# Performance work log

Measured on AMD Instinct MI355X. Metric: run time of the kernel, lower is better.

## Reference

```python
import jax, jax.numpy as jnp
import numpy as np

NUM_JOINTS = 24
V = 6890
# standard SMPL kinematic tree (parent of joint i); index 0 is the root
PARENTS = [-1, 0, 0, 0, 1, 2, 3, 4, 5, 6, 7, 8, 9, 9, 9, 12, 13, 14, 16, 17, 18, 19, 20, 21]


def rodrigues(r):
    """Axis-angle [.., 3] -> rotation matrices [.., 3, 3] (batched Rodrigues)."""
    angle = jnp.sqrt(jnp.sum(r * r, axis=-1, keepdims=True) + 1e-16)
    axis = r / angle
    c = jnp.cos(angle)[..., None]
    s = jnp.sin(angle)[..., None]
    x, y, z = axis[..., 0], axis[..., 1], axis[..., 2]
    zeros = jnp.zeros_like(x)
    K = jnp.stack([zeros, -z, y, z, zeros, -x, -y, x, zeros], axis=-1).reshape(r.shape[:-1] + (3, 3))
    outer = axis[..., :, None] * axis[..., None, :]
    eye = jnp.eye(3, dtype=r.dtype)
    return c * eye + (1.0 - c) * outer + s * K


def with_zeros(Rt):
    """[B,3,4] -> [B,4,4] homogeneous transform."""
    B = Rt.shape[0]
    bottom = jnp.broadcast_to(jnp.array([0.0, 0.0, 0.0, 1.0], Rt.dtype), (B, 1, 4))
    return jnp.concatenate([Rt, bottom], axis=1)


def setup_inputs() -> dict:
    key = jax.random.key(0)
    ks = jax.random.split(key, 8)
    B = 1024
    return {
        "pose": jax.random.normal(ks[0], (B, 72), jnp.float32) * 0.3,
        "betas": jax.random.normal(ks[1], (B, 10), jnp.float32),
        "trans": jax.random.normal(ks[2], (B, 3), jnp.float32),
        "v_template": jax.random.normal(ks[3], (V, 3), jnp.float32),
        "shapedirs": jax.random.normal(ks[4], (V, 3, 10), jnp.float32) * 0.01,
        "posedirs": jax.random.normal(ks[5], (V, 3, 207), jnp.float32) * 0.01,
        "J_regressor": jax.random.uniform(ks[6], (24, V), jnp.float32) / V,
        "weights": jax.random.uniform(ks[7], (V, 24), jnp.float32),
    }


def reference(pose, betas, trans, v_template, shapedirs, posedirs, J_regressor, weights):
    B = pose.shape[0]
    dt = pose.dtype
    # pose -> per-joint rotation matrices [B,24,3,3]
    rot = rodrigues(pose.reshape(B, NUM_JOINTS, 3))
    root_rot = rot[:, 0]
    # pose blendshape features: non-root rotations minus identity, flattened [B,207]
    pose_map = (rot[:, 1:] - jnp.eye(3, dtype=dt)).reshape(B, (NUM_JOINTS - 1) * 9)
    v_shaped = v_template[None] + jnp.einsum('vcs,bs->bvc', shapedirs, betas)   # [B,V,3]
    j = jnp.einsum('jv,bvc->bjc', J_regressor, v_shaped)                        # [B,24,3]
    naked = v_shaped + jnp.einsum('vcp,bp->bvc', posedirs, pose_map)            # [B,V,3]
    v_posed = naked  # th_offsets is None
    # forward kinematics along the fixed 24-joint tree
    results = [None] * NUM_JOINTS
    results[0] = with_zeros(jnp.concatenate([root_rot, j[:, 0, :, None]], axis=2))
    for i in range(1, NUM_JOINTS):
        p = PARENTS[i]
        rel = with_zeros(jnp.concatenate([rot[:, i], (j[:, i] - j[:, p])[:, :, None]], axis=2))
        results[i] = results[p] @ rel
    G = jnp.stack(results, axis=1)  # [B,24,4,4] global transforms
    # remove rest-pose joint locations: G_rel = G - pack(G @ [j;0])
    j_h = jnp.concatenate([j, jnp.zeros((B, NUM_JOINTS, 1), dt)], axis=-1)      # [B,24,4]
    tmp = jnp.einsum('bjpq,bjq->bjp', G, j_h)                                   # [B,24,4]
    G_rel = G - jnp.concatenate([jnp.zeros(G.shape[:-1] + (3,), dt), tmp[..., None]], axis=-1)
    # linear blend skinning
    T = jnp.einsum('bjpq,vj->bpqv', G_rel, weights)                              # [B,4,4,V]
    rest_h = jnp.concatenate(
        [v_posed.transpose(0, 2, 1), jnp.ones((B, 1, v_posed.shape[1]), dt)], axis=1)  # [B,4,V]
    verts = jnp.einsum('bpqv,bqv->bvp', T, rest_h)[:, :, :3]                     # [B,V,3]
    jtr = G[:, :, :3, 3]                                                         # [B,24,3]
    # scale=1.0, normalise=False
    verts = verts + trans[:, None]
    jtr = jtr + trans[:, None]
    return verts, jtr, v_posed, naked, G
```

## Files before the change

### kernel.cpp

```cpp
#include <hip/hip_runtime.h>
#include <math.h>

#define V_NUM 6890
#define NJ 24
#define KTOT 217
#define KP 256
#define M_DIM (V_NUM * 3)
#define MPAD 20736
#define VPAD 6912

typedef __attribute__((ext_vector_type(8))) short bf16x8;
typedef __attribute__((ext_vector_type(4))) float f32x4;

__constant__ int c_parents[NJ] = {-1,0,0,0,1,2,3,4,5,6,7,8,9,9,9,12,13,14,16,17,18,19,20,21};

__device__ __forceinline__ unsigned short f2bf(float x) {
  union { float f; unsigned int u; } v; v.f = x;
  unsigned int r = v.u + 0x7fffu + ((v.u >> 16) & 1u);
  return (unsigned short)(r >> 16);
}

#define GLOBAL_AS __attribute__((address_space(1)))
#define LDS_AS __attribute__((address_space(3)))
__device__ __forceinline__ void gl_lds16(const void* g, void* l) {
  __builtin_amdgcn_global_load_lds((const GLOBAL_AS unsigned int*)g,
                                   (LDS_AS unsigned int*)l, 16, 0, 0);
}

__global__ __launch_bounds__(256) void k_regress2(
    const float* __restrict__ JR, const float* __restrict__ SD,
    const float* __restrict__ VT, float* __restrict__ JS, float* __restrict__ Jt) {
  int j = blockIdx.x;
  int q = blockIdx.y;
  int tid = threadIdx.x;
  float part = 0.f;
  const float* jr = JR + (size_t)j * V_NUM;
  if (q < 30) {
    for (int v = tid; v < V_NUM; v += 256)
      part += jr[v] * SD[(size_t)v * 30 + q];
  } else {
    int cc = q - 30;
    for (int v = tid; v < V_NUM; v += 256)
      part += jr[v] * VT[(size_t)v * 3 + cc];
  }
  for (int off = 32; off > 0; off >>= 1) part += __shfl_down(part, off);
  __shared__ float sm[4];
  if ((tid & 63) == 0) sm[tid >> 6] = part;
  __syncthreads();
  if (tid == 0) {
    float s = sm[0] + sm[1] + sm[2] + sm[3];
    if (q < 30) JS[j * 30 + q] = s;
    else Jt[j * 3 + (q - 30)] = s;
  }
}

__global__ __launch_bounds__(256) void k_conv(
    const float* __restrict__ SD, const float* __restrict__ PD,
    const float* __restrict__ W,
    unsigned short* __restrict__ Abf, unsigned short* __restrict__ Wbf) {
  int bid = blockIdx.x;
  int tid = threadIdx.x;
  if (bid < MPAD) {
    int m = bid, k = tid;
    float v = 0.f;
    if (m < M_DIM && k < KTOT)
      v = (k < 10) ? SD[(size_t)m * 10 + k] : PD[(size_t)m * 207 + (k - 10)];
    Abf[(size_t)m * KP + k] = f2bf(v);
  } else {
    int idx = (bid - MPAD) * 256 + tid;
    if (idx < VPAD * 32) {
      int v = idx >> 5, k = idx & 31;
      Wbf[idx] = (v < V_NUM && k < NJ) ? f2bf(W[(size_t)v * NJ + k]) : (unsigned short)0;
    }
  }
}

__global__ __launch_bounds__(64) void k_batch(
    const float* __restrict__ pose, const float* __restrict__ betas,
    const float* __restrict__ trans, const float* __restrict__ JS,
    const float* __restrict__ Jt, unsigned short* __restrict__ Kcb,
    unsigned short* __restrict__ GrelP, float* __restrict__ outG,
    float* __restrict__ outJtr, int B) {
  int b = blockIdx.x;
  int lane = threadIdx.x;
  __shared__ float rotS[NJ][9];
  __shared__ float jS[NJ * 3];
  __shared__ float Gs[NJ][12];
  __shared__ float GrS[NJ][12];

  if (lane < NJ) {
    float rx = pose[b * 72 + lane * 3 + 0];
    float ry = pose[b * 72 + lane * 3 + 1];
    float rz = pose[b * 72 + lane * 3 + 2];
    float a2 = rx * rx + ry * ry + rz * rz + 1e-16f;
    float ang = sqrtf(a2);
    float inv = 1.f / ang;
    float ux = rx * inv, uy = ry * inv, uz = rz * inv;
    float c = cosf(ang), s = sinf(ang), ic = 1.f - c;
    float R[9];
    R[0] = c + ic * ux * ux;      R[1] = ic * ux * uy - s * uz; R[2] = ic * ux * uz + s * uy;
    R[3] = ic * uy * ux + s * uz; R[4] = c + ic * uy * uy;      R[5] = ic * uy * uz - s * ux;
    R[6] = ic * uz * ux - s * uy; R[7] = ic * uz * uy + s * ux; R[8] = c + ic * uz * uz;
#pragma unroll
    for (int k = 0; k < 9; k++) rotS[lane][k] = R[k];
    if (lane > 0) {
#pragma unroll
      for (int k = 0; k < 9; k++) {
        float iden = (k == 0 || k == 4 || k == 8) ? 1.f : 0.f;
        Kcb[(size_t)b * KP + 10 + (lane - 1) * 9 + k] = f2bf(R[k] - iden);
      }
    }
  }
  if (lane < 10) Kcb[(size_t)b * KP + lane] = f2bf(betas[b * 10 + lane]);
  if (lane < KP - KTOT) Kcb[(size_t)b * KP + KTOT + lane] = 0;

  __syncthreads();
  for (int idx = lane; idx < 72; idx += 64) {
    float s = Jt[idx];
#pragma unroll
    for (int ss = 0; ss < 10; ss++) s += JS[idx * 10 + ss] * betas[b * 10 + ss];
    jS[idx] = s;
  }
  __syncthreads();

  if (lane == 0) {
#pragma unroll
    for (int p = 0; p < 3; p++) {
      Gs[0][p * 4 + 0] = rotS[0][p * 3 + 0];
      Gs[0][p * 4 + 1] = rotS[0][p * 3 + 1];
      Gs[0][p * 4 + 2] = rotS[0][p * 3 + 2];
      Gs[0][p * 4 + 3] = jS[p];
    }
    for (int i = 1; i < NJ; i++) {
      int par = c_parents[i];
      float t0 = jS[i * 3 + 0] - jS[par * 3 + 0];
      float t1 = jS[i * 3 + 1] - jS[par * 3 + 1];
      float t2 = jS[i * 3 + 2] - jS[par * 3 + 2];
#pragma unroll
      for (int p = 0; p < 3; p++) {
        float rp0 = Gs[par][p * 4 + 0], rp1 = Gs[par][p * 4 + 1], rp2 = Gs[par][p * 4 + 2];
#pragma unroll
        for (int q = 0; q < 3; q++) {
          Gs[i][p * 4 + q] = rp0 * rotS[i][0 * 3 + q] + rp1 * rotS[i][1 * 3 + q] + rp2 * rotS[i][2 * 3 + q];
        }
        Gs[i][p * 4 + 3] = rp0 * t0 + rp1 * t1 + rp2 * t2 + Gs[par][p * 4 + 3];
      }
    }
    for (int i = 0; i < NJ; i++) {
      float jx = jS[i * 3 + 0], jy = jS[i * 3 + 1], jz = jS[i * 3 + 2];
#pragma unroll
      for (int p = 0; p < 3; p++) {
        float g0 = Gs[i][p * 4 + 0], g1 = Gs[i][p * 4 + 1], g2 = Gs[i][p * 4 + 2];
        GrS[i][p * 4 + 0] = g0;
        GrS[i][p * 4 + 1] = g1;
        GrS[i][p * 4 + 2] = g2;
        GrS[i][p * 4 + 3] = Gs[i][p * 4 + 3] - (g0 * jx + g1 * jy + g2 * jz);
      }
    }
  }
  __syncthreads();

  for (int idx = lane; idx < NJ * 16; idx += 64) {
    int jj = idx >> 4, rc = idx & 15, p = rc >> 2, q = rc & 3;
    float val = (p < 3) ? Gs[jj][p * 4 + q] : ((q == 3) ? 1.f : 0.f);
    outG[(size_t)b * NJ * 16 + idx] = val;
  }
  for (int idx = lane; idx < NJ * 3; idx += 64) {
    int jj = idx / 3, p = idx % 3;
    outJtr[(size_t)b * NJ * 3 + idx] = Gs[jj][p * 4 + 3] + trans[b * 3 + p];
  }
  for (int idx = lane; idx < 16 * 40; idx += 64) {
    int c = idx / 40, j = idx % 40;
    GrelP[(size_t)b * 640 + idx] = (c < 12 && j < NJ) ? f2bf(GrS[j][c]) : (unsigned short)0;
  }
}

__global__ __launch_bounds__(256) void k_pose_mfma(
    const unsigned short* __restrict__ Kcb, const unsigned short* __restrict__ Abf,
    const float* __restrict__ VT, float* __restrict__ outVP, int B) {
  __shared__ char ldsraw[32768];

  const int tid = threadIdx.x;
  const int lane = tid & 63;
  const int w = tid >> 6;
  const int wr = w >> 1, wc = w & 1;
  const int b0 = blockIdx.y * 128;
  const int m0 = blockIdx.x * 128;

  f32x4 vt4[4];
  {
    int mbase = m0 + wr * 64 + ((lane >> 4) << 4);
#pragma unroll
    for (int i = 0; i < 4; i++) {
      int mm = mbase + i * 4;
      if (mm + 3 < M_DIM) vt4[i] = *(const f32x4*)(VT + mm);
      else {
#pragma unroll
        for (int r = 0; r < 4; r++) vt4[i][r] = (mm + r < M_DIM) ? VT[mm + r] : 0.f;
      }
    }
  }

  f32x4 acc[4][4];
#pragma unroll
  for (int i = 0; i < 4; i++)
#pragma unroll
    for (int j = 0; j < 4; j++) acc[i][j] = (f32x4){0.f, 0.f, 0.f, 0.f};

  int Lrow[4], Lkb[4];
#pragma unroll
  for (int i = 0; i < 4; i++) {
    int L = w * 4096 + i * 1024 + lane * 16;
    int row = L >> 7;
    int kb = (L & 127) ^ ((row & 7) << 4);
    Lrow[i] = row;
    Lkb[i] = kb >> 1;
  }

#pragma unroll
  for (int kt = 0; kt < 4; ++kt) {
    char* At = ldsraw;
    char* Bt = ldsraw + 16384;
#pragma unroll
    for (int i = 0; i < 4; i++) {
      const unsigned short* gA = Kcb + (size_t)(b0 + Lrow[i]) * KP + kt * 64 + Lkb[i];
      gl_lds16(gA, At + w * 4096 + i * 1024);
      const unsigned short* gB = Abf + (size_t)(m0 + Lrow[i]) * KP + kt * 64 + Lkb[i];
      gl_lds16(gB, Bt + w * 4096 + i * 1024);
    }
    __syncthreads();
#pragma unroll
    for (int h = 0; h < 2; ++h) {
      bf16x8 fm[4], fb[4];
#pragma unroll
      for (int fi = 0; fi < 4; fi++) {
        int row = wr * 64 + fi * 16 + (lane & 15);
        int byte = (row << 7) + ((h * 64 + ((lane >> 4) << 4)) ^ ((row & 7) << 4));
        fm[fi] = *(const bf16x8*)(Bt + byte);
      }
#pragma unroll
      for (int fj = 0; fj < 4; fj++) {
        int row = wc * 64 + fj * 16 + (lane & 15);
        int byte = (row << 7) + ((h * 64 + ((lane >> 4) << 4)) ^ ((row & 7) << 4));
        fb[fj] = *(const bf16x8*)(At + byte);
      }
#pragma unroll
      for (int fi = 0; fi < 4; fi++)
#pragma unroll
        for (int fj = 0; fj < 4; fj++)
          acc[fi][fj] = __builtin_amdgcn_mfma_f32_16x16x32_bf16(fm[fi], fb[fj], acc[fi][fj], 0, 0, 0);
    }
    __syncthreads();
  }

  char* wslab = ldsraw + w * 4352;
  const int a = lane & 15, c = lane >> 4;
  const int xr = (lane & 3) << 4;
#pragma unroll
  for (int fj = 0; fj < 4; fj++) {
#pragma unroll
    for (int fi = 0; fi < 4; fi++) {
      int off = a * 272 + (((fi << 6) + (c << 4)) ^ xr);
      *(f32x4*)(wslab + off) = acc[fi][fj];
    }
    int brow = b0 + wc * 64 + fj * 16 + a;
    size_t gb = (size_t)brow * M_DIM;
    int mg0 = m0 + wr * 64 + (c << 4);
#pragma unroll
    for (int i = 0; i < 4; i++) {
      int off = a * 272 + (((c << 6) + (i << 4)) ^ xr);
      f32x4 v = *(f32x4*)(wslab + off);
      v = v + vt4[i];
      int mg = mg0 + i * 4;
      if (mg + 3 < M_DIM) {
        *(f32x4*)(outVP + gb + mg) = v;
      } else {
#pragma unroll
        for (int r = 0; r < 4; r++)
          if (mg + r < M_DIM) outVP[gb + mg + r] = v[r];
      }
    }
  }
}

__global__ __launch_bounds__(256) void k_skin9(
    const float* __restrict__ VP, const unsigned short* __restrict__ Wbf,
    const unsigned short* __restrict__ GrelP, const float* __restrict__ trans,
    float* __restrict__ outNK, float* __restrict__ outVerts, int B) {
  __shared__ float Tl[4][64 * 16];
  const int tid = threadIdx.x;
  const int lane = tid & 63;
  const int w = tid >> 6;
  const int vl16 = lane & 15;
  const int p = lane >> 4;
  const int kb = p * 8;
  const int vbase = blockIdx.x * 256 + w * 64;
  const int b0 = blockIdx.y * 4;
  const int vg = vbase + lane;
  const bool vok = vg < V_NUM;
  const int kx = (lane >> 1) & 3;

  bf16x8 wf[4];
#pragma unroll
  for (int sub = 0; sub < 4; sub++)
    wf[sub] = *(const bf16x8*)(Wbf + (size_t)(vbase + sub * 16 + vl16) * 32 + kb);

  bf16x8 af[4];
#pragma unroll
  for (int bi = 0; bi < 4; bi++)
    af[bi] = *(const bf16x8*)(GrelP + (size_t)(b0 + bi) * 640 + vl16 * 40 + kb);

  float* myT = Tl[w];

  float xc0 = 0.f, xc1 = 0.f, xc2 = 0.f;
  if (vok) {
    const float* xp = VP + (size_t)b0 * M_DIM + (size_t)vg * 3;
    xc0 = xp[0]; xc1 = xp[1]; xc2 = xp[2];
  }

#pragma unroll
  for (int bi = 0; bi < 4; bi++) {
    int b = b0 + bi;
    f32x4 acc[4];
#pragma unroll
    for (int sub = 0; sub < 4; sub++) {
      f32x4 z = (f32x4){0.f, 0.f, 0.f, 0.f};
      acc[sub] = __builtin_amdgcn_mfma_f32_16x16x32_bf16(af[bi], wf[sub], z, 0, 0, 0);
    }
#pragma unroll
    for (int sub = 0; sub < 4; sub++) {
      int vi = sub * 16 + vl16;
      int slot = p ^ ((vi >> 1) & 3);
      *(f32x4*)&myT[vi * 16 + slot * 4] = acc[sub];
    }
    float xn0 = 0.f, xn1 = 0.f, xn2 = 0.f;
    if (bi < 3 && vok) {
      const float* xp = VP + (size_t)(b + 1) * M_DIM + (size_t)vg * 3;
      xn0 = xp[0]; xn1 = xp[1]; xn2 = xp[2];
    }
    if (vok) {
      f32x4 ta = *(f32x4*)&myT[lane * 16 + ((0 ^ kx) << 2)];
      f32x4 tb = *(f32x4*)&myT[lane * 16 + ((1 ^ kx) << 2)];
      f32x4 tc = *(f32x4*)&myT[lane * 16 + ((2 ^ kx) << 2)];
      size_t base = (size_t)b * M_DIM + (size_t)vg * 3;
      float* onk = outNK + base;
      onk[0] = xc0; onk[1] = xc1; onk[2] = xc2;
      float* op = outVerts + base;
      op[0] = ta[0] * xc0 + ta[1] * xc1 + ta[2] * xc2 + ta[3] + trans[b * 3 + 0];
      op[1] = tb[0] * xc0 + tb[1] * xc1 + tb[2] * xc2 + tb[3] + trans[b * 3 + 1];
      op[2] = tc[0] * xc0 + tc[1] * xc1 + tc[2] * xc2 + tc[3] + trans[b * 3 + 2];
    }
    xc0 = xn0; xc1 = xn1; xc2 = xn2;
  }
}

extern "C" void kernel_launch(void* const* d_in, const int* in_sizes, int n_in,
                              void* d_out, int out_size, void* d_ws, size_t ws_size,
                              hipStream_t stream) {
  const float* pose  = (const float*)d_in[0];
  const float* betas = (const float*)d_in[1];
  const float* trans = (const float*)d_in[2];
  const float* vt    = (const float*)d_in[3];
  const float* sd    = (const float*)d_in[4];
  const float* pd    = (const float*)d_in[5];
  const float* jreg  = (const float*)d_in[6];
  const float* wgt   = (const float*)d_in[7];
  int B = in_sizes[0] / 72;

  float* out = (float*)d_out;
  size_t nvb = (size_t)B * M_DIM;
  float* o_verts = out;
  float* o_jtr   = o_verts + nvb;
  float* o_vp    = o_jtr + (size_t)B * NJ * 3;
  float* o_nk    = o_vp + nvb;
  float* o_G     = o_nk + nvb;

  char* wsb = (char*)d_ws;
  float* JS = (float*)wsb;
  float* Jt = JS + 720;
  size_t off = (720 + 72) * 4;
  unsigned short* Kcb   = (unsigned short*)(wsb + off);
  unsigned short* Abf   = (unsigned short*)(wsb + off + (size_t)B * KP * 2);
  unsigned short* GrelP = Abf + (size_t)MPAD * KP;
  unsigned short* Wbf   = GrelP + (size_t)B * 640;

  dim3 gR(24, 33);
  k_regress2<<<gR, 256, 0, stream>>>(jreg, sd, vt, JS, Jt);
  k_conv<<<MPAD + (VPAD * 32 + 255) / 256, 256, 0, stream>>>(sd, pd, wgt, Abf, Wbf);
  k_batch<<<B, 64, 0, stream>>>(pose, betas, trans, JS, Jt, Kcb, GrelP, o_G, o_jtr, B);
  dim3 gC(MPAD / 128, B / 128);
  k_pose_mfma<<<gC, 256, 0, stream>>>(Kcb, Abf, vt, o_vp, B);
  dim3 gD(VPAD / 256, B / 4);
  k_skin9<<<gD, 256, 0, stream>>>(o_vp, Wbf, GrelP, trans, o_nk, o_verts, B);
}
```

Before: 149.2 us.

## Fuse pose-blendshape GEMM with skinning to avoid re-reading v_posed

Merges the pose-blendshape MFMA GEMM and the skinning kernel into one kernel. Each block now covers 192 output columns (64 vertices × 3) by 128 batches, stages the v_posed tile in LDS, and runs skinning directly from it. This removes the global round-trip of v_posed: it is written once but never read back, and one launch is dropped. In exchange the kernel uses 64KB of LDS and more accumulators per thread, which lowers occupancy. The skinning stores are strided 3-float writes and sit in a serial per-batch loop.

```diff
diff --git a/kernel.cpp b/kernel.cpp
--- a/kernel.cpp
+++ b/kernel.cpp
@@ -175,182 +175,164 @@
   }
 }
 
-__global__ __launch_bounds__(256) void k_pose_mfma(
+__global__ __launch_bounds__(256) void k_fused(
     const unsigned short* __restrict__ Kcb, const unsigned short* __restrict__ Abf,
-    const float* __restrict__ VT, float* __restrict__ outVP, int B) {
-  __shared__ char ldsraw[32768];
-
+    const float* __restrict__ VT, const unsigned short* __restrict__ Wbf,
+    const unsigned short* __restrict__ GrelP, const float* __restrict__ trans,
+    float* __restrict__ outVP, float* __restrict__ outNK,
+    float* __restrict__ outVerts, int B) {
+  __shared__ char ldsraw[65536];
   const int tid = threadIdx.x;
   const int lane = tid & 63;
   const int w = tid >> 6;
   const int wr = w >> 1, wc = w & 1;
   const int b0 = blockIdx.y * 128;
-  const int m0 = blockIdx.x * 128;
-
-  f32x4 vt4[4];
-  {
-    int mbase = m0 + wr * 64 + ((lane >> 4) << 4);
-#pragma unroll
-    for (int i = 0; i < 4; i++) {
-      int mm = mbase + i * 4;
-      if (mm + 3 < M_DIM) vt4[i] = *(const f32x4*)(VT + mm);
-      else {
-#pragma unroll
-        for (int r = 0; r < 4; r++) vt4[i][r] = (mm + r < M_DIM) ? VT[mm + r] : 0.f;
-      }
-    }
-  }
-
-  f32x4 acc[4][4];
-#pragma unroll
-  for (int i = 0; i < 4; i++)
-#pragma unroll
-    for (int j = 0; j < 4; j++) acc[i][j] = (f32x4){0.f, 0.f, 0.f, 0.f};
-
-  int Lrow[4], Lkb[4];
-#pragma unroll
-  for (int i = 0; i < 4; i++) {
-    int L = w * 4096 + i * 1024 + lane * 16;
-    int row = L >> 7;
-    int kb = (L & 127) ^ ((row & 7) << 4);
-    Lrow[i] = row;
-    Lkb[i] = kb >> 1;
-  }
-
-#pragma unroll
-  for (int kt = 0; kt < 4; ++kt) {
-    char* At = ldsraw;
-    char* Bt = ldsraw + 16384;
-#pragma unroll
-    for (int i = 0; i < 4; i++) {
-      const unsigned short* gA = Kcb + (size_t)(b0 + Lrow[i]) * KP + kt * 64 + Lkb[i];
-      gl_lds16(gA, At + w * 4096 + i * 1024);
-      const unsigned short* gB = Abf + (size_t)(m0 + Lrow[i]) * KP + kt * 64 + Lkb[i];
-      gl_lds16(gB, Bt + w * 4096 + i * 1024);
-    }
-    __syncthreads();
-#pragma unroll
-    for (int h = 0; h < 2; ++h) {
-      bf16x8 fm[4], fb[4];
-#pragma unroll
-      for (int fi = 0; fi < 4; fi++) {
-        int row = wr * 64 + fi * 16 + (lane & 15);
-        int byte = (row << 7) + ((h * 64 + ((lane >> 4) << 4)) ^ ((row & 7) << 4));
-        fm[fi] = *(const bf16x8*)(Bt + byte);
-      }
-#pragma unroll
-      for (int fj = 0; fj < 4; fj++) {
-        int row = wc * 64 + fj * 16 + (lane & 15);
-        int byte = (row << 7) + ((h * 64 + ((lane >> 4) << 4)) ^ ((row & 7) << 4));
-        fb[fj] = *(const bf16x8*)(At + byte);
-      }
-#pragma unroll
-      for (int fi = 0; fi < 4; fi++)
-#pragma unroll
-        for (int fj = 0; fj < 4; fj++)
-          acc[fi][fj] = __builtin_amdgcn_mfma_f32_16x16x32_bf16(fm[fi], fb[fj], acc[fi][fj], 0, 0, 0);
-    }
-    __syncthreads();
-  }
-
-  char* wslab = ldsraw + w * 4352;
-  const int a = lane & 15, c = lane >> 4;
-  const int xr = (lane & 3) << 4;
-#pragma unroll
-  for (int fj = 0; fj < 4; fj++) {
-#pragma unroll
-    for (int fi = 0; fi < 4; fi++) {
-      int off = a * 272 + (((fi << 6) + (c << 4)) ^ xr);
-      *(f32x4*)(wslab + off) = acc[fi][fj];
-    }
-    int brow = b0 + wc * 64 + fj * 16 + a;
-    size_t gb = (size_t)brow * M_DIM;
-    int mg0 = m0 + wr * 64 + (c << 4);
-#pragma unroll
-    for (int i = 0; i < 4; i++) {
-      int off = a * 272 + (((c << 6) + (i << 4)) ^ xr);
-      f32x4 v = *(f32x4*)(wslab + off);
-      v = v + vt4[i];
-      int mg = mg0 + i * 4;
-      if (mg + 3 < M_DIM) {
-        *(f32x4*)(outVP + gb + mg) = v;
-      } else {
-#pragma unroll
-        for (int r = 0; r < 4; r++)
-          if (mg + r < M_DIM) outVP[gb + mg + r] = v[r];
-      }
-    }
-  }
-}
-
-__global__ __launch_bounds__(256) void k_skin9(
-    const float* __restrict__ VP, const unsigned short* __restrict__ Wbf,
-    const unsigned short* __restrict__ GrelP, const float* __restrict__ trans,
-    float* __restrict__ outNK, float* __restrict__ outVerts, int B) {
-  __shared__ float Tl[4][64 * 16];
-  const int tid = threadIdx.x;
-  const int lane = tid & 63;
-  const int w = tid >> 6;
+  const int m0 = blockIdx.x * 192;
+  const int v0 = blockIdx.x * 64;
   const int vl16 = lane & 15;
   const int p = lane >> 4;
   const int kb = p * 8;
-  const int vbase = blockIdx.x * 256 + w * 64;
-  const int b0 = blockIdx.y * 4;
-  const int vg = vbase + lane;
+
+  bf16x8 wf[4];
+#pragma unroll
+  for (int sub = 0; sub < 4; sub++)
+    wf[sub] = *(const bf16x8*)(Wbf + (size_t)(v0 + sub * 16 + vl16) * 32 + kb);
+
+  f32x4 vt4[6];
+#pragma unroll
+  for (int fi = 0; fi < 6; fi++) {
+    int mm = m0 + wr * 96 + fi * 16 + ((lane >> 4) << 2);
+    if (mm + 3 < M_DIM) vt4[fi] = *(const f32x4*)(VT + mm);
+    else {
+#pragma unroll
+      for (int r = 0; r < 4; r++) vt4[fi][r] = (mm + r < M_DIM) ? VT[mm + r] : 0.f;
+    }
+  }
+
+  f32x4 acc[6][4];
+#pragma unroll
+  for (int i = 0; i < 6; i++)
+#pragma unroll
+    for (int j = 0; j < 4; j++) acc[i][j] = (f32x4){0.f, 0.f, 0.f, 0.f};
+
+  int LrowA[4], LkbA[4], LrowB[6], LkbB[6];
+#pragma unroll
+  for (int i = 0; i < 4; i++) {
+    int L = (w * 4 + i) * 1024 + lane * 16;
+    int row = L >> 7;
+    int kk = (L & 127) ^ ((row & 7) << 4);
+    LrowA[i] = row; LkbA[i] = kk >> 1;
+  }
+#pragma unroll
+  for (int i = 0; i < 6; i++) {
+    int L = (w * 6 + i) * 1024 + lane * 16;
+    int row = L >> 7;
+    int kk = (L & 127) ^ ((row & 7) << 4);
+    LrowB[i] = row; LkbB[i] = kk >> 1;
+  }
+
+  char* At = ldsraw;
+  char* Bt = ldsraw + 16384;
+
+#pragma unroll
+  for (int kt = 0; kt < 4; ++kt) {
+#pragma unroll
+    for (int i = 0; i < 4; i++)
+      gl_lds16(Kcb + (size_t)(b0 + LrowA[i]) * KP + kt * 64 + LkbA[i],
+               At + (w * 4 + i) * 1024);
+#pragma unroll
+    for (int i = 0; i < 6; i++)
+      gl_lds16(Abf + (size_t)(m0 + LrowB[i]) * KP + kt * 64 + LkbB[i],
+               Bt + (w * 6 + i) * 1024);
+    __syncthreads();
+#pragma unroll
+    for (int hh = 0; hh < 2; ++hh) {
+      bf16x8 fm[6], fb[4];
+#pragma unroll
+      for (int fi = 0; fi < 6; fi++) {
+        int row = wr * 96 + fi * 16 + vl16;
+        int byte = (row << 7) + ((hh * 64 + ((lane >> 4) << 4)) ^ ((row & 7) << 4));
+        fm[fi] = *(const bf16x8*)(Bt + byte);
+      }
+#pragma unroll
+      for (int fj = 0; fj < 4; fj++) {
+        int row = wc * 64 + fj * 16 + vl16;
+        int byte = (row << 7) + ((hh * 64 + ((lane >> 4) << 4)) ^ ((row & 7) << 4));
+        fb[fj] = *(const bf16x8*)(At + byte);
+      }
+#pragma unroll
+      for (int fi = 0; fi < 6; fi++)
+#pragma unroll
+        for (int fj = 0; fj < 4; fj++)
+          acc[fi][fj] = __builtin_amdgcn_mfma_f32_16x16x32_bf16(fm[fi], fb[fj], acc[fi][fj], 0, 0, 0);
+    }
+    __syncthreads();
+  }
+
+#pragma unroll
+  for (int fi = 0; fi < 6; fi++)
+#pragma unroll
+    for (int fj = 0; fj < 4; fj++) acc[fi][fj] = acc[fi][fj] + vt4[fi];
+
+  char* xslab = ldsraw;
+  float* Tslab = (float*)(ldsraw + 49152);
+  float* myT = Tslab + w * 1024;
+  const int vg = v0 + lane;
   const bool vok = vg < V_NUM;
   const int kx = (lane >> 1) & 3;
 
-  bf16x8 wf[4];
-#pragma unroll
-  for (int sub = 0; sub < 4; sub++)
-    wf[sub] = *(const bf16x8*)(Wbf + (size_t)(vbase + sub * 16 + vl16) * 32 + kb);
-
-  bf16x8 af[4];
-#pragma unroll
-  for (int bi = 0; bi < 4; bi++)
-    af[bi] = *(const bf16x8*)(GrelP + (size_t)(b0 + bi) * 640 + vl16 * 40 + kb);
-
-  float* myT = Tl[w];
-
-  float xc0 = 0.f, xc1 = 0.f, xc2 = 0.f;
-  if (vok) {
-    const float* xp = VP + (size_t)b0 * M_DIM + (size_t)vg * 3;
-    xc0 = xp[0]; xc1 = xp[1]; xc2 = xp[2];
-  }
-
-#pragma unroll
-  for (int bi = 0; bi < 4; bi++) {
-    int b = b0 + bi;
-    f32x4 acc[4];
-#pragma unroll
-    for (int sub = 0; sub < 4; sub++) {
-      f32x4 z = (f32x4){0.f, 0.f, 0.f, 0.f};
-      acc[sub] = __builtin_amdgcn_mfma_f32_16x16x32_bf16(af[bi], wf[sub], z, 0, 0, 0);
-    }
-#pragma unroll
-    for (int sub = 0; sub < 4; sub++) {
-      int vi = sub * 16 + vl16;
-      int slot = p ^ ((vi >> 1) & 3);
-      *(f32x4*)&myT[vi * 16 + slot * 4] = acc[sub];
-    }
-    float xn0 = 0.f, xn1 = 0.f, xn2 = 0.f;
-    if (bi < 3 && vok) {
-      const float* xp = VP + (size_t)(b + 1) * M_DIM + (size_t)vg * 3;
-      xn0 = xp[0]; xn1 = xp[1]; xn2 = xp[2];
-    }
-    if (vok) {
-      f32x4 ta = *(f32x4*)&myT[lane * 16 + ((0 ^ kx) << 2)];
-      f32x4 tb = *(f32x4*)&myT[lane * 16 + ((1 ^ kx) << 2)];
-      f32x4 tc = *(f32x4*)&myT[lane * 16 + ((2 ^ kx) << 2)];
-      size_t base = (size_t)b * M_DIM + (size_t)vg * 3;
-      float* onk = outNK + base;
-      onk[0] = xc0; onk[1] = xc1; onk[2] = xc2;
-      float* op = outVerts + base;
-      op[0] = ta[0] * xc0 + ta[1] * xc1 + ta[2] * xc2 + ta[3] + trans[b * 3 + 0];
-      op[1] = tb[0] * xc0 + tb[1] * xc1 + tb[2] * xc2 + tb[3] + trans[b * 3 + 1];
-      op[2] = tc[0] * xc0 + tc[1] * xc1 + tc[2] * xc2 + tc[3] + trans[b * 3 + 2];
-    }
-    xc0 = xn0; xc1 = xn1; xc2 = xn2;
+#pragma unroll
+  for (int h = 0; h < 2; ++h) {
+    __syncthreads();
+    if (wc == h) {
+#pragma unroll
+      for (int fj = 0; fj < 4; fj++) {
+        int brow = fj * 16 + vl16;
+        int xorv = (brow & 7) << 4;
+#pragma unroll
+        for (int fi = 0; fi < 6; fi++) {
+          int mbyte = (wr * 384) + (fi << 6) + ((lane >> 4) << 4);
+          *(f32x4*)(xslab + brow * 768 + (mbyte ^ xorv)) = acc[fi][fj];
+        }
+      }
+    }
+    __syncthreads();
+    for (int bi = 0; bi < 16; ++bi) {
+      int bloc = w * 16 + bi;
+      int gb = b0 + h * 64 + bloc;
+      bf16x8 af = *(const bf16x8*)(GrelP + (size_t)gb * 640 + vl16 * 40 + kb);
+      f32x4 t[4];
+#pragma unroll
+      for (int sub = 0; sub < 4; sub++) {
+        f32x4 z = (f32x4){0.f, 0.f, 0.f, 0.f};
+        t[sub] = __builtin_amdgcn_mfma_f32_16x16x32_bf16(af, wf[sub], z, 0, 0, 0);
+      }
+#pragma unroll
+      for (int sub = 0; sub < 4; sub++) {
+        int vi = sub * 16 + vl16;
+        int slot = p ^ ((vi >> 1) & 3);
+        *(f32x4*)&myT[vi * 16 + slot * 4] = t[sub];
+      }
+      int xk = (bloc & 7) << 4;
+      const char* rowp = xslab + bloc * 768;
+      float x0 = *(const float*)(rowp + ((lane * 12 + 0) ^ xk));
+      float x1 = *(const float*)(rowp + ((lane * 12 + 4) ^ xk));
+      float x2 = *(const float*)(rowp + ((lane * 12 + 8) ^ xk));
+      if (vok) {
+        f32x4 ta = *(const f32x4*)&myT[lane * 16 + ((0 ^ kx) << 2)];
+        f32x4 tb = *(const f32x4*)&myT[lane * 16 + ((1 ^ kx) << 2)];
+        f32x4 tc = *(const f32x4*)&myT[lane * 16 + ((2 ^ kx) << 2)];
+        size_t base = (size_t)gb * M_DIM + (size_t)vg * 3;
+        float* ovp = outVP + base;
+        ovp[0] = x0; ovp[1] = x1; ovp[2] = x2;
+        float* onk = outNK + base;
+        onk[0] = x0; onk[1] = x1; onk[2] = x2;
+        float* op = outVerts + base;
+        op[0] = ta[0] * x0 + ta[1] * x1 + ta[2] * x2 + ta[3] + trans[gb * 3 + 0];
+        op[1] = tb[0] * x0 + tb[1] * x1 + tb[2] * x2 + tb[3] + trans[gb * 3 + 1];
+        op[2] = tc[0] * x0 + tc[1] * x1 + tc[2] * x2 + tc[3] + trans[gb * 3 + 2];
+      }
+    }
   }
 }
 
@@ -388,8 +370,6 @@
   k_regress2<<<gR, 256, 0, stream>>>(jreg, sd, vt, JS, Jt);
   k_conv<<<MPAD + (VPAD * 32 + 255) / 256, 256, 0, stream>>>(sd, pd, wgt, Abf, Wbf);
   k_batch<<<B, 64, 0, stream>>>(pose, betas, trans, JS, Jt, Kcb, GrelP, o_G, o_jtr, B);
-  dim3 gC(MPAD / 128, B / 128);
-  k_pose_mfma<<<gC, 256, 0, stream>>>(Kcb, Abf, vt, o_vp, B);
-  dim3 gD(VPAD / 256, B / 4);
-  k_skin9<<<gD, 256, 0, stream>>>(o_vp, Wbf, GrelP, trans, o_nk, o_verts, B);
-}
+  dim3 gF(MPAD / 192, B / 128);
+  k_fused<<<gF, 256, 0, stream>>>(Kcb, Abf, vt, Wbf, GrelP, trans, o_vp, o_nk, o_verts, B);
+}
```

Result: slower. 167.6 us (+12.3%).
